# Kernel optimization log

Hardware: AMD Instinct MI355X
Metric: run time of the kernel (lower is better)

Reference implementation:

```python
import jax, jax.numpy as jnp
import numpy as np

NEG_SLOPE = 0.2  # PyG GATConv default negative_slope
EPS = 1e-16


def gat_conv(x, src, dst, num_nodes, W, att_src, att_dst, bias, concat):
    """PyG-style GATConv (eval mode, no dropout). att_*: [H, C]."""
    H, C = att_src.shape
    h = (x @ W).reshape(num_nodes, H, C)                      # [N,H,C]
    a_s = jnp.einsum('nhc,hc->nh', h, att_src)                # [N,H]
    a_d = jnp.einsum('nhc,hc->nh', h, att_dst)                # [N,H]
    e = jax.nn.leaky_relu(a_s[src] + a_d[dst], NEG_SLOPE)     # [E,H]
    # segment softmax over edges grouped by destination node
    m = jax.lax.stop_gradient(jax.ops.segment_max(e, dst, num_segments=num_nodes))
    ex = jnp.exp(e - m[dst])
    denom = jax.ops.segment_sum(ex, dst, num_segments=num_nodes)
    alpha = ex / (denom[dst] + EPS)                           # [E,H]
    msg = h[src] * alpha[:, :, None]                          # [E,H,C]
    out = jax.ops.segment_sum(msg, dst, num_segments=num_nodes)  # [N,H,C]
    out = out.reshape(num_nodes, H * C) if concat else out.mean(axis=1)
    return out + bias


def setup_inputs() -> dict:
    key = jax.random.key(0)
    ks = jax.random.split(key, 12)
    N, E = 65536, 1310720
    IN, HID, OUT, HEADS = 768, 128, 2, 8
    C1 = HID // HEADS  # 16
    s = 0.05
    return {
        'x': jax.random.normal(ks[0], (N, IN), jnp.float32),
        'edge_index': jax.random.randint(ks[1], (2, E), 0, N, jnp.int64),
        'W1': jax.random.normal(ks[2], (IN, HEADS * C1), jnp.float32) * s,
        'att_src1': jax.random.normal(ks[3], (HEADS, C1), jnp.float32) * s,
        'att_dst1': jax.random.normal(ks[4], (HEADS, C1), jnp.float32) * s,
        'b1': jnp.zeros((HID,), jnp.float32),
        'Wp': jax.random.normal(ks[5], (IN, HID), jnp.float32) * s,
        'bp': jnp.zeros((HID,), jnp.float32),
        'W2': jax.random.normal(ks[6], (HID, OUT), jnp.float32) * s,
        'att_src2': jax.random.normal(ks[7], (1, OUT), jnp.float32) * s,
        'att_dst2': jax.random.normal(ks[8], (1, OUT), jnp.float32) * s,
        'b2': jnp.zeros((OUT,), jnp.float32),
    }


def reference(x, edge_index, W1, att_src1, att_dst1, b1, Wp, bp, W2, att_src2, att_dst2, b2):
    N = x.shape[0]
    loops = jnp.arange(N, dtype=edge_index.dtype)  # add_self_loops=True
    src = jnp.concatenate([edge_index[0], loops])
    dst = jnp.concatenate([edge_index[1], loops])
    # eval mode: dropout is identity
    h1 = gat_conv(x, src, dst, N, W1, att_src1, att_dst1, b1, concat=True)
    h = jax.nn.elu(h1 + x @ Wp + bp)  # residual projection + ELU
    return gat_conv(h, src, dst, N, W2, att_src2, att_dst2, b2, concat=False)
```

## Files before the change

kernel.cpp:

```cpp
#include <hip/hip_runtime.h>
#include <hip/hip_bf16.h>
#include <math.h>

#define NEG_SLOPE 0.2f

typedef __attribute__((ext_vector_type(8))) short short8;
typedef __attribute__((ext_vector_type(4))) float float4v;

__device__ __forceinline__ unsigned f2bf(float f) {
  unsigned u = __builtin_bit_cast(unsigned, f);
  return (u + 0x7fffu + ((u >> 16) & 1u)) >> 16;
}
__device__ __forceinline__ float bflo(unsigned u) {
  return __builtin_bit_cast(float, u << 16);
}
__device__ __forceinline__ float bfhi(unsigned u) {
  return __builtin_bit_cast(float, u & 0xffff0000u);
}
__device__ __forceinline__ unsigned cvtpk(float lo, float hi) {
  unsigned r;
  asm("v_cvt_pk_bf16_f32 %0, %1, %2" : "=v"(r) : "v"(lo), "v"(hi));
  return r;
}
__device__ __forceinline__ void gl2lds16(const void* g, void* l) {
  __builtin_amdgcn_global_load_lds(
      (const __attribute__((address_space(1))) unsigned*)g,
      (__attribute__((address_space(3))) unsigned*)l, 16, 0, 0);
}

__global__ __launch_bounds__(256) void convert_w(const float* __restrict__ W1,
                                                 const float* __restrict__ Wp,
                                                 short* __restrict__ Wt) {
  int k = blockIdx.x;
  int c = threadIdx.x;
  float v = (c < 128) ? W1[k * 128 + c] : Wp[k * 128 + (c - 128)];
  Wt[(size_t)c * 768 + k] = (short)f2bf(v);
}

__global__ __launch_bounds__(512, 4) void gemm_mfma(
    const float* __restrict__ x, const short* __restrict__ Wt,
    float* __restrict__ proj, unsigned* __restrict__ h1bf) {
  __shared__ short As[2][4096];
  __shared__ short Bs[2][8192];
  const int tid = threadIdx.x;
  const int w = tid >> 6, l = tid & 63;
  const int wr = w >> 2, wc = w & 3;
  const int l15 = l & 15, l4 = l >> 4;
  const int row0 = blockIdx.x * 128;

  const float* xsrc = x + (size_t)(row0 + (tid >> 2)) * 768 + (tid & 3) * 8;
  const int awoff = (tid >> 2) * 64 + (((tid & 3) ^ ((tid >> 3) & 3)) << 4);
  const int aoff = (wr * 64 + l15) * 64 + ((l4 ^ ((l15 >> 1) & 3)) << 4);

  const char* bg[2];
#pragma unroll
  for (int i = 0; i < 2; i++) {
    int c = w * 32 + i * 16 + (l >> 2);
    int q = (l & 3) ^ ((l >> 3) & 3);
    bg[i] = (const char*)Wt + (size_t)c * 1536 + q * 16;
  }
  const int pc = l4 ^ ((l15 >> 1) & 3);

  float4v acc[4][4] = {};

  auto loadA = [&](int t, float4& r0, float4& r1) {
    const float* p = xsrc + t * 32;
    r0 = *(const float4*)p;
    r1 = *(const float4*)(p + 4);
  };
  auto writeA = [&](short* asb, const float4& r0, const float4& r1) {
    uint4 pk;
    pk.x = cvtpk(r0.x, r0.y);
    pk.y = cvtpk(r0.z, r0.w);
    pk.z = cvtpk(r1.x, r1.y);
    pk.w = cvtpk(r1.z, r1.w);
    *(uint4*)((char*)asb + awoff) = pk;
  };
  auto stageB = [&](short* bsb, int t) {
    gl2lds16(bg[0] + t * 64, (char*)bsb + w * 2048 + 0 * 1024);
    gl2lds16(bg[1] + t * 64, (char*)bsb + w * 2048 + 1 * 1024);
  };
  auto compute = [&](const short* asb, const short* bsb) {
    short8 afr[4];
#pragma unroll
    for (int rt = 0; rt < 4; rt++)
      afr[rt] = *(const short8*)((const char*)asb + rt * 1024 + aoff);
#pragma unroll
    for (int ct = 0; ct < 4; ct++) {
      short8 bfr =
          *(const short8*)((const char*)bsb + (wc * 64 + ct * 16 + l15) * 64 + pc * 16);
#pragma unroll
      for (int rt = 0; rt < 4; rt++)
        acc[rt][ct] =
            __builtin_amdgcn_mfma_f32_16x16x32_bf16(afr[rt], bfr, acc[rt][ct], 0, 0, 0);
    }
  };
  auto pub_barrier = [&]() {
    asm volatile("s_waitcnt vmcnt(2)" ::: "memory");
    asm volatile("s_waitcnt lgkmcnt(0)" ::: "memory");
    __builtin_amdgcn_sched_barrier(0);
    __builtin_amdgcn_s_barrier();
    __builtin_amdgcn_sched_barrier(0);
  };

  float4 p0, p1, q0, q1;
  loadA(0, p0, p1);
  __builtin_amdgcn_sched_barrier(0);
  stageB(Bs[0], 0);
  __builtin_amdgcn_sched_barrier(0);
  loadA(1, q0, q1);
  __builtin_amdgcn_sched_barrier(0);
  writeA(As[0], p0, p1);
  pub_barrier();

  for (int t = 0; t < 22; t += 2) {
    stageB(Bs[1], t + 1);
    __builtin_amdgcn_sched_barrier(0);
    loadA(t + 2, p0, p1);
    __builtin_amdgcn_sched_barrier(0);
    compute(As[0], Bs[0]);
    writeA(As[1], q0, q1);
    pub_barrier();
    stageB(Bs[0], t + 2);
    __builtin_amdgcn_sched_barrier(0);
    loadA(t + 3, q0, q1);
    __builtin_amdgcn_sched_barrier(0);
    compute(As[1], Bs[1]);
    writeA(As[0], p0, p1);
    pub_barrier();
  }
  stageB(Bs[1], 23);
  __builtin_amdgcn_sched_barrier(0);
  compute(As[0], Bs[0]);
  writeA(As[1], q0, q1);
  asm volatile("s_waitcnt vmcnt(0)" ::: "memory");
  asm volatile("s_waitcnt lgkmcnt(0)" ::: "memory");
  __builtin_amdgcn_sched_barrier(0);
  __builtin_amdgcn_s_barrier();
  __builtin_amdgcn_sched_barrier(0);
  compute(As[1], Bs[1]);

  if (wc < 2) {
#pragma unroll
    for (int ct = 0; ct < 4; ct++) {
      const int c = wc * 64 + ct * 16 + l15;
#pragma unroll
      for (int rt = 0; rt < 4; rt++) {
#pragma unroll
        for (int r = 0; r < 4; r++) {
          const int R = row0 + wr * 64 + rt * 16 + l4 * 4 + r;
          unsigned u = f2bf(acc[rt][ct][r]);
          unsigned up = __shfl_xor(u, 1);
          if ((l15 & 1) == 0) h1bf[(size_t)R * 64 + (c >> 1)] = u | (up << 16);
        }
      }
    }
  } else {
#pragma unroll
    for (int ct = 0; ct < 4; ct++) {
      const int c = (wc - 2) * 64 + ct * 16 + l15;
#pragma unroll
      for (int rt = 0; rt < 4; rt++) {
#pragma unroll
        for (int r = 0; r < 4; r++) {
          const int R = row0 + wr * 64 + rt * 16 + l4 * 4 + r;
          proj[(size_t)R * 128 + c] = acc[rt][ct][r];
        }
      }
    }
  }
}

__global__ __launch_bounds__(256) void attn1b(const uint4* __restrict__ h1bf4,
                                              const float* __restrict__ att_src1,
                                              const float* __restrict__ att_dst1,
                                              float* __restrict__ a_s1,
                                              float* __restrict__ a_d1) {
  const int t = blockIdx.x * 256 + threadIdx.x;
  const int n = t >> 3, h = t & 7;
  uint4 q0 = h1bf4[(size_t)n * 16 + h * 2];
  uint4 q1 = h1bf4[(size_t)n * 16 + h * 2 + 1];
  float v[16];
  v[0] = bflo(q0.x); v[1] = bfhi(q0.x); v[2] = bflo(q0.y); v[3] = bfhi(q0.y);
  v[4] = bflo(q0.z); v[5] = bfhi(q0.z); v[6] = bflo(q0.w); v[7] = bfhi(q0.w);
  v[8] = bflo(q1.x); v[9] = bfhi(q1.x); v[10] = bflo(q1.y); v[11] = bfhi(q1.y);
  v[12] = bflo(q1.z); v[13] = bfhi(q1.z); v[14] = bflo(q1.w); v[15] = bfhi(q1.w);
  float as = 0.f, ad = 0.f;
#pragma unroll
  for (int i = 0; i < 16; i++) {
    as += v[i] * att_src1[h * 16 + i];
    ad += v[i] * att_dst1[h * 16 + i];
  }
  a_s1[t] = as;
  a_d1[t] = ad;
}

__global__ void init_counts(int* counts, int N) {
  int i = blockIdx.x * blockDim.x + threadIdx.x;
  if (i < N) counts[i] = 1;
}

__global__ void hist_kernel(const int* __restrict__ dst, int* counts,
                            int* __restrict__ rank, int E) {
  int i = blockIdx.x * blockDim.x + threadIdx.x;
  int base = i * 4;
  if (base + 3 < E) {
    int4 d = *(const int4*)&dst[base];
    int4 r;
    r.x = atomicAdd(&counts[d.x], 1);
    r.y = atomicAdd(&counts[d.y], 1);
    r.z = atomicAdd(&counts[d.z], 1);
    r.w = atomicAdd(&counts[d.w], 1);
    *(int4*)&rank[base] = r;
  } else {
    for (int j = base; j < E; j++) rank[j] = atomicAdd(&counts[dst[j]], 1);
  }
}

__global__ __launch_bounds__(256) void scan_a(const int* __restrict__ counts,
                                              int* offsets, int* bsum) {
  __shared__ int s[256];
  int t = threadIdx.x, idx = blockIdx.x * 256 + t;
  int v = counts[idx];
  s[t] = v;
  __syncthreads();
  for (int d = 1; d < 256; d <<= 1) {
    int x = (t >= d) ? s[t - d] : 0;
    __syncthreads();
    s[t] += x;
    __syncthreads();
  }
  offsets[idx] = s[t] - v;
  if (t == 255) bsum[blockIdx.x] = s[t];
}

__global__ __launch_bounds__(256) void scan_b(int* bsum) {
  __shared__ int s[256];
  int t = threadIdx.x;
  int v = bsum[t];
  s[t] = v;
  __syncthreads();
  for (int d = 1; d < 256; d <<= 1) {
    int x = (t >= d) ? s[t - d] : 0;
    __syncthreads();
    s[t] += x;
    __syncthreads();
  }
  bsum[t] = s[t] - v;
}

__global__ __launch_bounds__(256) void scan_c(int* offsets, const int* bsum,
                                              int* sortedsrc, int N, int Etot) {
  int t = threadIdx.x, idx = blockIdx.x * 256 + t;
  int off = offsets[idx] + bsum[blockIdx.x];
  offsets[idx] = off;
  sortedsrc[off] = idx;
  if (idx == 0) offsets[N] = Etot;
}

__global__ void scatter_edges(const int* __restrict__ src,
                              const int* __restrict__ dst,
                              const int* __restrict__ rank,
                              const int* __restrict__ offsets,
                              int* __restrict__ sortedsrc, int E) {
  int i = blockIdx.x * blockDim.x + threadIdx.x;
  int base = i * 4;
  if (base + 3 < E) {
    int4 s = *(const int4*)&src[base];
    int4 d = *(const int4*)&dst[base];
    int4 r = *(const int4*)&rank[base];
    sortedsrc[offsets[d.x] + r.x] = s.x;
    sortedsrc[offsets[d.y] + r.y] = s.y;
    sortedsrc[offsets[d.z] + r.z] = s.z;
    sortedsrc[offsets[d.w] + r.w] = s.w;
  } else {
    for (int j = base; j < E; j++)
      sortedsrc[offsets[dst[j]] + rank[j]] = src[j];
  }
}

__global__ __launch_bounds__(256) void agg1_fused(
    const uint4* __restrict__ h1bf4, const float* __restrict__ proj,
    const float* __restrict__ a_s1, const float* __restrict__ a_d1,
    const int* __restrict__ offsets, const int* __restrict__ sortedsrc,
    const float* __restrict__ b1, const float* __restrict__ bp,
    const float* __restrict__ W2, const float* __restrict__ att_s2,
    const float* __restrict__ att_d2, float4* __restrict__ rec) {
  const int t = threadIdx.x;
  const int n = blockIdx.x * 16 + (t >> 4);
  const int k = t & 15;
  const int hd = k >> 1;
  const float ad = a_d1[n * 8 + hd];
  const int begin = offsets[n], end = offsets[n + 1];
  float acc[8] = {};
  float aw = 0.f;
  int j = begin;
  for (; j + 4 <= end; j += 4) {
    int s0 = sortedsrc[j], s1 = sortedsrc[j + 1];
    int s2 = sortedsrc[j + 2], s3 = sortedsrc[j + 3];
    float e0 = a_s1[s0 * 8 + hd], e1 = a_s1[s1 * 8 + hd];
    float e2 = a_s1[s2 * 8 + hd], e3 = a_s1[s3 * 8 + hd];
    uint4 q0 = h1bf4[(size_t)s0 * 16 + k];
    uint4 q1 = h1bf4[(size_t)s1 * 16 + k];
    uint4 q2 = h1bf4[(size_t)s2 * 16 + k];
    uint4 q3 = h1bf4[(size_t)s3 * 16 + k];
    e0 += ad; e1 += ad; e2 += ad; e3 += ad;
    float w0 = __expf(e0 > 0.f ? e0 : NEG_SLOPE * e0);
    float w1 = __expf(e1 > 0.f ? e1 : NEG_SLOPE * e1);
    float w2 = __expf(e2 > 0.f ? e2 : NEG_SLOPE * e2);
    float w3 = __expf(e3 > 0.f ? e3 : NEG_SLOPE * e3);
    acc[0] += w0 * bflo(q0.x) + w1 * bflo(q1.x) + w2 * bflo(q2.x) + w3 * bflo(q3.x);
    acc[1] += w0 * bfhi(q0.x) + w1 * bfhi(q1.x) + w2 * bfhi(q2.x) + w3 * bfhi(q3.x);
    acc[2] += w0 * bflo(q0.y) + w1 * bflo(q1.y) + w2 * bflo(q2.y) + w3 * bflo(q3.y);
    acc[3] += w0 * bfhi(q0.y) + w1 * bfhi(q1.y) + w2 * bfhi(q2.y) + w3 * bfhi(q3.y);
    acc[4] += w0 * bflo(q0.z) + w1 * bflo(q1.z) + w2 * bflo(q2.z) + w3 * bflo(q3.z);
    acc[5] += w0 * bfhi(q0.z) + w1 * bfhi(q1.z) + w2 * bfhi(q2.z) + w3 * bfhi(q3.z);
    acc[6] += w0 * bflo(q0.w) + w1 * bflo(q1.w) + w2 * bflo(q2.w) + w3 * bflo(q3.w);
    acc[7] += w0 * bfhi(q0.w) + w1 * bfhi(q1.w) + w2 * bfhi(q2.w) + w3 * bfhi(q3.w);
    aw += (w0 + w1) + (w2 + w3);
  }
  for (; j < end; j++) {
    int s0 = sortedsrc[j];
    float e0 = a_s1[s0 * 8 + hd] + ad;
    uint4 q0 = h1bf4[(size_t)s0 * 16 + k];
    float w0 = __expf(e0 > 0.f ? e0 : NEG_SLOPE * e0);
    acc[0] += w0 * bflo(q0.x);
    acc[1] += w0 * bfhi(q0.x);
    acc[2] += w0 * bflo(q0.y);
    acc[3] += w0 * bfhi(q0.y);
    acc[4] += w0 * bflo(q0.z);
    acc[5] += w0 * bfhi(q0.z);
    acc[6] += w0 * bflo(q0.w);
    acc[7] += w0 * bfhi(q0.w);
    aw += w0;
  }
  const float inv = 1.f / (aw + 1e-16f);
  const float4 pj0 = *(const float4*)&proj[(size_t)n * 128 + k * 8];
  const float4 pj1 = *(const float4*)&proj[(size_t)n * 128 + k * 8 + 4];
  const float4 b1a = *(const float4*)&b1[k * 8];
  const float4 b1b = *(const float4*)&b1[k * 8 + 4];
  const float4 bpa = *(const float4*)&bp[k * 8];
  const float4 bpb = *(const float4*)&bp[k * 8 + 4];
  float v[8];
  v[0] = acc[0] * inv + pj0.x + b1a.x + bpa.x;
  v[1] = acc[1] * inv + pj0.y + b1a.y + bpa.y;
  v[2] = acc[2] * inv + pj0.z + b1a.z + bpa.z;
  v[3] = acc[3] * inv + pj0.w + b1a.w + bpa.w;
  v[4] = acc[4] * inv + pj1.x + b1b.x + bpb.x;
  v[5] = acc[5] * inv + pj1.y + b1b.y + bpb.y;
  v[6] = acc[6] * inv + pj1.z + b1b.z + bpb.z;
  v[7] = acc[7] * inv + pj1.w + b1b.w + bpb.w;
  float p0 = 0.f, p1 = 0.f;
#pragma unroll
  for (int i = 0; i < 8; i++) {
    float vi = v[i] > 0.f ? v[i] : (__expf(v[i]) - 1.f);
    float2 w2 = *(const float2*)&W2[(k * 8 + i) * 2];
    p0 += vi * w2.x;
    p1 += vi * w2.y;
  }
#pragma unroll
  for (int off = 8; off; off >>= 1) {
    p0 += __shfl_xor(p0, off);
    p1 += __shfl_xor(p1, off);
  }
  if (k == 0) {
    float as = p0 * att_s2[0] + p1 * att_s2[1];
    float adv = p0 * att_d2[0] + p1 * att_d2[1];
    rec[n] = make_float4(p0, p1, as, adv);
  }
}

__global__ __launch_bounds__(256) void agg2(
    const float4* __restrict__ rec, const int* __restrict__ offsets,
    const int* __restrict__ sortedsrc, const float* __restrict__ b2,
    float* __restrict__ out, int N) {
  const int node = blockIdx.x * 16 + (threadIdx.x >> 4);
  const int lane = threadIdx.x & 15;
  const int begin = offsets[node], end = offsets[node + 1];
  const float ad = rec[node].w;
  float acc0 = 0.f, acc1 = 0.f, aw = 0.f;
  for (int j = begin + lane; j < end; j += 16) {
    int s = sortedsrc[j];
    float4 rs = rec[s];
    float e = rs.z + ad;
    float w = __expf(e > 0.f ? e : NEG_SLOPE * e);
    acc0 += w * rs.x;
    acc1 += w * rs.y;
    aw += w;
  }
#pragma unroll
  for (int off = 8; off; off >>= 1) {
    acc0 += __shfl_xor(acc0, off);
    acc1 += __shfl_xor(acc1, off);
    aw += __shfl_xor(aw, off);
  }
  if (lane == 0) {
    float inv = 1.f / (aw + 1e-16f);
    out[2 * node] = acc0 * inv + b2[0];
    out[2 * node + 1] = acc1 * inv + b2[1];
  }
}

extern "C" void kernel_launch(void* const* d_in, const int* in_sizes, int n_in,
                              void* d_out, int out_size, void* d_ws,
                              size_t ws_size, hipStream_t stream) {
  const float* x = (const float*)d_in[0];
  const int* edge_index = (const int*)d_in[1];
  const float* W1 = (const float*)d_in[2];
  const float* att_src1 = (const float*)d_in[3];
  const float* att_dst1 = (const float*)d_in[4];
  const float* b1 = (const float*)d_in[5];
  const float* Wp = (const float*)d_in[6];
  const float* bp = (const float*)d_in[7];
  const float* W2 = (const float*)d_in[8];
  const float* att_src2 = (const float*)d_in[9];
  const float* att_dst2 = (const float*)d_in[10];
  const float* b2 = (const float*)d_in[11];
  float* out = (float*)d_out;

  const int N = in_sizes[0] / 768;
  const int E = in_sizes[1] / 2;
  const int Etot = E + N;
  const int* src = edge_index;
  const int* dst = edge_index + E;

  char* ws = (char*)d_ws;
  size_t off = 0;
  auto alloc = [&](size_t bytes) {
    size_t cur = off;
    off += (bytes + 255) & ~(size_t)255;
    return (void*)(ws + cur);
  };
  float* proj = (float*)alloc((size_t)N * 128 * 4);
  unsigned* h1bf = (unsigned*)alloc((size_t)N * 64 * 4);
  float* a_s1 = (float*)alloc((size_t)N * 8 * 4);
  float* a_d1 = (float*)alloc((size_t)N * 8 * 4);
  float4* rec = (float4*)alloc((size_t)N * 16);
  int* counts = (int*)alloc((size_t)N * 4);
  int* offsets = (int*)alloc(((size_t)N + 1) * 4);
  int* rank = (int*)alloc((size_t)E * 4);
  int* bsum = (int*)alloc(256 * 4);
  int* sortedsrc = (int*)alloc((size_t)Etot * 4);
  short* Wt = (short*)alloc((size_t)256 * 768 * 2);

  convert_w<<<768, 256, 0, stream>>>(W1, Wp, Wt);
  gemm_mfma<<<N / 128, 512, 0, stream>>>(x, Wt, proj, h1bf);
  attn1b<<<N * 8 / 256, 256, 0, stream>>>((const uint4*)h1bf, att_src1,
                                          att_dst1, a_s1, a_d1);
  init_counts<<<(N + 255) / 256, 256, 0, stream>>>(counts, N);
  hist_kernel<<<(E / 4 + 255) / 256, 256, 0, stream>>>(dst, counts, rank, E);
  scan_a<<<N / 256, 256, 0, stream>>>(counts, offsets, bsum);
  scan_b<<<1, 256, 0, stream>>>(bsum);
  scan_c<<<N / 256, 256, 0, stream>>>(offsets, bsum, sortedsrc, N, Etot);
  scatter_edges<<<(E / 4 + 255) / 256, 256, 0, stream>>>(src, dst, rank,
                                                         offsets, sortedsrc, E);
  agg1_fused<<<N / 16, 256, 0, stream>>>((const uint4*)h1bf, proj, a_s1, a_d1,
                                         offsets, sortedsrc, b1, bp, W2,
                                         att_src2, att_dst2, rec);
  agg2<<<N / 16, 256, 0, stream>>>(rec, offsets, sortedsrc, b2, out, N);
}
```

Measured before the change: 493.7 us.

## Split layer-1 aggregation into per-head passes with head-major attention scores

Layer-1 aggregation now runs as eight separate launches, one per head, and attention scores are stored head-major. The goal is a per-pass gather working set (one 32-byte slice of h1 per source plus one score array) small enough to stay in cache. Each pass accumulates its partial layer-2 projection into a two-float record via non-atomic read-modify-write, so the passes depend on launch ordering. Layer-2 attention logits are now recomputed in agg2 from the two-float record instead of being stored, which shrinks the record from 16 to 8 bytes. The cost is eight gathers over the edge list and two threads per node per pass, which reduces parallelism per launch.

```diff
diff --git a/kernel.cpp b/kernel.cpp
--- a/kernel.cpp
+++ b/kernel.cpp
@@ -175,7 +175,7 @@
                                               const float* __restrict__ att_src1,
                                               const float* __restrict__ att_dst1,
                                               float* __restrict__ a_s1,
-                                              float* __restrict__ a_d1) {
+                                              float* __restrict__ a_d1, int N) {
   const int t = blockIdx.x * 256 + threadIdx.x;
   const int n = t >> 3, h = t & 7;
   uint4 q0 = h1bf4[(size_t)n * 16 + h * 2];
@@ -191,13 +191,17 @@
     as += v[i] * att_src1[h * 16 + i];
     ad += v[i] * att_dst1[h * 16 + i];
   }
-  a_s1[t] = as;
-  a_d1[t] = ad;
-}
-
-__global__ void init_counts(int* counts, int N) {
+  a_s1[(size_t)h * N + n] = as;
+  a_d1[(size_t)h * N + n] = ad;
+}
+
+__global__ void init_counts(int* counts, float* recf, int N) {
   int i = blockIdx.x * blockDim.x + threadIdx.x;
-  if (i < N) counts[i] = 1;
+  if (i < N) {
+    counts[i] = 1;
+    recf[2 * i] = 0.f;
+    recf[2 * i + 1] = 0.f;
+  }
 }
 
 __global__ void hist_kernel(const int* __restrict__ dst, int* counts,
@@ -279,18 +283,18 @@
   }
 }
 
-__global__ __launch_bounds__(256) void agg1_fused(
+__global__ __launch_bounds__(256) void agg1_pass(
     const uint4* __restrict__ h1bf4, const float* __restrict__ proj,
-    const float* __restrict__ a_s1, const float* __restrict__ a_d1,
+    const float* __restrict__ a_s1h, const float* __restrict__ a_d1h,
     const int* __restrict__ offsets, const int* __restrict__ sortedsrc,
     const float* __restrict__ b1, const float* __restrict__ bp,
-    const float* __restrict__ W2, const float* __restrict__ att_s2,
-    const float* __restrict__ att_d2, float4* __restrict__ rec) {
+    const float* __restrict__ W2, float* __restrict__ recf, int hp, int N) {
   const int t = threadIdx.x;
-  const int n = blockIdx.x * 16 + (t >> 4);
-  const int k = t & 15;
-  const int hd = k >> 1;
-  const float ad = a_d1[n * 8 + hd];
+  const int n = blockIdx.x * 128 + (t >> 1);
+  const int k = t & 1;
+  const float* as1 = a_s1h + (size_t)hp * N;
+  const float ad = a_d1h[(size_t)hp * N + n];
+  const int qoff = hp * 2 + k;
   const int begin = offsets[n], end = offsets[n + 1];
   float acc[8] = {};
   float aw = 0.f;
@@ -298,12 +302,11 @@
   for (; j + 4 <= end; j += 4) {
     int s0 = sortedsrc[j], s1 = sortedsrc[j + 1];
     int s2 = sortedsrc[j + 2], s3 = sortedsrc[j + 3];
-    float e0 = a_s1[s0 * 8 + hd], e1 = a_s1[s1 * 8 + hd];
-    float e2 = a_s1[s2 * 8 + hd], e3 = a_s1[s3 * 8 + hd];
-    uint4 q0 = h1bf4[(size_t)s0 * 16 + k];
-    uint4 q1 = h1bf4[(size_t)s1 * 16 + k];
-    uint4 q2 = h1bf4[(size_t)s2 * 16 + k];
-    uint4 q3 = h1bf4[(size_t)s3 * 16 + k];
+    float e0 = as1[s0], e1 = as1[s1], e2 = as1[s2], e3 = as1[s3];
+    uint4 q0 = h1bf4[(size_t)s0 * 16 + qoff];
+    uint4 q1 = h1bf4[(size_t)s1 * 16 + qoff];
+    uint4 q2 = h1bf4[(size_t)s2 * 16 + qoff];
+    uint4 q3 = h1bf4[(size_t)s3 * 16 + qoff];
     e0 += ad; e1 += ad; e2 += ad; e3 += ad;
     float w0 = __expf(e0 > 0.f ? e0 : NEG_SLOPE * e0);
     float w1 = __expf(e1 > 0.f ? e1 : NEG_SLOPE * e1);
@@ -321,8 +324,8 @@
   }
   for (; j < end; j++) {
     int s0 = sortedsrc[j];
-    float e0 = a_s1[s0 * 8 + hd] + ad;
-    uint4 q0 = h1bf4[(size_t)s0 * 16 + k];
+    float e0 = as1[s0] + ad;
+    uint4 q0 = h1bf4[(size_t)s0 * 16 + qoff];
     float w0 = __expf(e0 > 0.f ? e0 : NEG_SLOPE * e0);
     acc[0] += w0 * bflo(q0.x);
     acc[1] += w0 * bfhi(q0.x);
@@ -335,12 +338,13 @@
     aw += w0;
   }
   const float inv = 1.f / (aw + 1e-16f);
-  const float4 pj0 = *(const float4*)&proj[(size_t)n * 128 + k * 8];
-  const float4 pj1 = *(const float4*)&proj[(size_t)n * 128 + k * 8 + 4];
-  const float4 b1a = *(const float4*)&b1[k * 8];
-  const float4 b1b = *(const float4*)&b1[k * 8 + 4];
-  const float4 bpa = *(const float4*)&bp[k * 8];
-  const float4 bpb = *(const float4*)&bp[k * 8 + 4];
+  const int cb = hp * 16 + k * 8;
+  const float4 pj0 = *(const float4*)&proj[(size_t)n * 128 + cb];
+  const float4 pj1 = *(const float4*)&proj[(size_t)n * 128 + cb + 4];
+  const float4 b1a = *(const float4*)&b1[cb];
+  const float4 b1b = *(const float4*)&b1[cb + 4];
+  const float4 bpa = *(const float4*)&bp[cb];
+  const float4 bpb = *(const float4*)&bp[cb + 4];
   float v[8];
   v[0] = acc[0] * inv + pj0.x + b1a.x + bpa.x;
   v[1] = acc[1] * inv + pj0.y + b1a.y + bpa.y;
@@ -354,35 +358,34 @@
 #pragma unroll
   for (int i = 0; i < 8; i++) {
     float vi = v[i] > 0.f ? v[i] : (__expf(v[i]) - 1.f);
-    float2 w2 = *(const float2*)&W2[(k * 8 + i) * 2];
+    float2 w2 = *(const float2*)&W2[(cb + i) * 2];
     p0 += vi * w2.x;
     p1 += vi * w2.y;
   }
-#pragma unroll
-  for (int off = 8; off; off >>= 1) {
-    p0 += __shfl_xor(p0, off);
-    p1 += __shfl_xor(p1, off);
-  }
+  p0 += __shfl_xor(p0, 1);
+  p1 += __shfl_xor(p1, 1);
   if (k == 0) {
-    float as = p0 * att_s2[0] + p1 * att_s2[1];
-    float adv = p0 * att_d2[0] + p1 * att_d2[1];
-    rec[n] = make_float4(p0, p1, as, adv);
+    recf[2 * n] += p0;
+    recf[2 * n + 1] += p1;
   }
 }
 
 __global__ __launch_bounds__(256) void agg2(
-    const float4* __restrict__ rec, const int* __restrict__ offsets,
+    const float2* __restrict__ rec2, const int* __restrict__ offsets,
     const int* __restrict__ sortedsrc, const float* __restrict__ b2,
+    const float* __restrict__ att_s2, const float* __restrict__ att_d2,
     float* __restrict__ out, int N) {
   const int node = blockIdx.x * 16 + (threadIdx.x >> 4);
   const int lane = threadIdx.x & 15;
   const int begin = offsets[node], end = offsets[node + 1];
-  const float ad = rec[node].w;
+  const float ws0 = att_s2[0], ws1 = att_s2[1];
+  float2 rn = rec2[node];
+  const float ad = rn.x * att_d2[0] + rn.y * att_d2[1];
   float acc0 = 0.f, acc1 = 0.f, aw = 0.f;
   for (int j = begin + lane; j < end; j += 16) {
     int s = sortedsrc[j];
-    float4 rs = rec[s];
-    float e = rs.z + ad;
+    float2 rs = rec2[s];
+    float e = rs.x * ws0 + rs.y * ws1 + ad;
     float w = __expf(e > 0.f ? e : NEG_SLOPE * e);
     acc0 += w * rs.x;
     acc1 += w * rs.y;
@@ -435,7 +438,7 @@
   unsigned* h1bf = (unsigned*)alloc((size_t)N * 64 * 4);
   float* a_s1 = (float*)alloc((size_t)N * 8 * 4);
   float* a_d1 = (float*)alloc((size_t)N * 8 * 4);
-  float4* rec = (float4*)alloc((size_t)N * 16);
+  float* recf = (float*)alloc((size_t)N * 8);
   int* counts = (int*)alloc((size_t)N * 4);
   int* offsets = (int*)alloc(((size_t)N + 1) * 4);
   int* rank = (int*)alloc((size_t)E * 4);
@@ -446,16 +449,18 @@
   convert_w<<<768, 256, 0, stream>>>(W1, Wp, Wt);
   gemm_mfma<<<N / 128, 512, 0, stream>>>(x, Wt, proj, h1bf);
   attn1b<<<N * 8 / 256, 256, 0, stream>>>((const uint4*)h1bf, att_src1,
-                                          att_dst1, a_s1, a_d1);
-  init_counts<<<(N + 255) / 256, 256, 0, stream>>>(counts, N);
+                                          att_dst1, a_s1, a_d1, N);
+  init_counts<<<(N + 255) / 256, 256, 0, stream>>>(counts, recf, N);
   hist_kernel<<<(E / 4 + 255) / 256, 256, 0, stream>>>(dst, counts, rank, E);
   scan_a<<<N / 256, 256, 0, stream>>>(counts, offsets, bsum);
   scan_b<<<1, 256, 0, stream>>>(bsum);
   scan_c<<<N / 256, 256, 0, stream>>>(offsets, bsum, sortedsrc, N, Etot);
   scatter_edges<<<(E / 4 + 255) / 256, 256, 0, stream>>>(src, dst, rank,
                                                          offsets, sortedsrc, E);
-  agg1_fused<<<N / 16, 256, 0, stream>>>((const uint4*)h1bf, proj, a_s1, a_d1,
-                                         offsets, sortedsrc, b1, bp, W2,
-                                         att_src2, att_dst2, rec);
-  agg2<<<N / 16, 256, 0, stream>>>(rec, offsets, sortedsrc, b2, out, N);
-}
+  for (int hp = 0; hp < 8; hp++)
+    agg1_pass<<<N / 128, 256, 0, stream>>>((const uint4*)h1bf, proj, a_s1,
+                                           a_d1, offsets, sortedsrc, b1, bp,
+                                           W2, recf, hp, N);
+  agg2<<<N / 16, 256, 0, stream>>>((const float2*)recf, offsets, sortedsrc,
+                                   b2, att_src2, att_dst2, out, N);
+}
```

Result: slower. 623.3 us (+26.2%).
